# Optimization experiments

Hardware: AMD Instinct MI355X
Metric: run time of the kernel (lower is better)

Reference implementation:

```python
import jax, jax.numpy as jnp
import numpy as np

N_EXPERTS = 8
TOP_K = 2


def setup_inputs() -> dict:
    key = jax.random.key(0)
    ks = jax.random.split(key, 6)
    x = jax.random.normal(ks[0], (4, 2048, 1024), dtype=jnp.float32)
    gate_w = jax.random.normal(ks[1], (8, 1024), dtype=jnp.float32) * 0.02
    w1 = jax.random.normal(ks[2], (8, 4096, 1024), dtype=jnp.float32) * 0.02
    b1 = jax.random.normal(ks[3], (8, 4096), dtype=jnp.float32) * 0.02
    w2 = jax.random.normal(ks[4], (8, 1024, 4096), dtype=jnp.float32) * 0.02
    b2 = jax.random.normal(ks[5], (8, 1024), dtype=jnp.float32) * 0.02
    return {"x": x, "gate_w": gate_w, "w1": w1, "b1": b1, "w2": w2, "b2": b2}


def reference(x, gate_w, w1, b1, w2, b2):
    B, N, C = x.shape
    flat = x.reshape(-1, C)                      # [T, C]
    T = flat.shape[0]
    # Router (eval mode: no noise)
    logits = flat @ gate_w.T                     # [T, E]
    probs = jax.nn.softmax(logits, axis=-1)
    top_p, top_i = jax.lax.top_k(probs, TOP_K)   # [T, K]
    weights = top_p / (jnp.sum(top_p, axis=-1, keepdims=True) + 1e-8)
    # Per-token combine weight per expert: sum_k weights[t,k] * [top_i[t,k]==e]
    combine = jnp.zeros((T, N_EXPERTS), dtype=flat.dtype)
    combine = combine.at[jnp.arange(T)[:, None], top_i].add(weights)  # [T, E]
    # Expert FFNs: small fixed loop over experts, masked-weighted combine.
    out = jnp.zeros_like(flat)
    for e in range(N_EXPERTS):
        h = jax.nn.gelu(flat @ w1[e].T + b1[e])  # [T, H]
        y = h @ w2[e].T + b2[e]                  # [T, C]
        out = out + combine[:, e:e + 1] * y
    return out.reshape(B, N, C)
```

## Files before the change

kernel.cpp:

```cpp
#include <hip/hip_runtime.h>
#include <math.h>

#define T_TOK 8192
#define CD 1024
#define HD 4096
#define NE 8
#define MAX_SLOTS 18432

#define BM 128
#define BN 128
#define BK 64
#define MSLOTS 64
#define G1_NB 32
#define G2_NB 8

typedef __bf16 bf16x8 __attribute__((ext_vector_type(8)));
typedef float f32x4 __attribute__((ext_vector_type(4)));

__device__ __forceinline__ unsigned short f2bf(float f) {
  union { float f; unsigned int u; } v; v.f = f;
  unsigned int u = v.u;
  return (unsigned short)((u + 0x7FFFu + ((u >> 16) & 1u)) >> 16);
}

__device__ __forceinline__ float gelu_fast(float x) {
  float x3 = x * x * x;
  float z = 0.7978845608028654f * (x + 0.044715f * x3);
  float ez = __expf(-2.0f * z);
  return x * __builtin_amdgcn_rcpf(1.0f + ez);
}

__device__ __forceinline__ void glds16(const void* g, void* l) {
  __builtin_amdgcn_global_load_lds((__attribute__((address_space(1))) void*)g,
                                   (__attribute__((address_space(3))) void*)l,
                                   16, 0, 0);
}

__global__ void router_kernel(const float* __restrict__ x, const float* __restrict__ gw,
                              int* __restrict__ meta, int* __restrict__ route_e,
                              float* __restrict__ route_w) {
  __shared__ float4 sgw4[NE * (CD / 4)];
  __shared__ int hist[NE];
  const int tid = threadIdx.x;
  for (int idx = tid; idx < NE * CD / 4; idx += 256) sgw4[idx] = ((const float4*)gw)[idx];
  if (tid < NE) hist[tid] = 0;
  __syncthreads();
  const int wave = tid >> 6, lane = tid & 63;
  const int t0 = blockIdx.x * 16 + wave * 4;
#pragma unroll
  for (int tt = 0; tt < 4; tt++) {
    const int t = t0 + tt;
    const float4* xr4 = (const float4*)(x + (size_t)t * CD);
    float4 xv[4];
#pragma unroll
    for (int it = 0; it < 4; it++) xv[it] = xr4[it * 64 + lane];
    float acc[NE];
#pragma unroll
    for (int e = 0; e < NE; e++) acc[e] = 0.f;
#pragma unroll
    for (int it = 0; it < 4; it++) {
#pragma unroll
      for (int e = 0; e < NE; e++) {
        float4 g = sgw4[e * 256 + it * 64 + lane];
        acc[e] += xv[it].x * g.x + xv[it].y * g.y + xv[it].z * g.z + xv[it].w * g.w;
      }
    }
#pragma unroll
    for (int e = 0; e < NE; e++) {
      float v = acc[e];
#pragma unroll
      for (int off = 32; off > 0; off >>= 1) v += __shfl_xor(v, off);
      acc[e] = v;
    }
    if (lane == 0) {
      float mx = acc[0];
#pragma unroll
      for (int e = 1; e < NE; e++) mx = fmaxf(mx, acc[e]);
      float p[NE], s = 0.f;
#pragma unroll
      for (int e = 0; e < NE; e++) { p[e] = __expf(acc[e] - mx); s += p[e]; }
      float inv = 1.0f / s;
#pragma unroll
      for (int e = 0; e < NE; e++) p[e] *= inv;
      int i0 = 0;
#pragma unroll
      for (int e = 1; e < NE; e++) if (p[e] > p[i0]) i0 = e;
      int i1 = (i0 == 0) ? 1 : 0;
#pragma unroll
      for (int e = 0; e < NE; e++) if (e != i0 && p[e] > p[i1]) i1 = e;
      float den = p[i0] + p[i1] + 1e-8f;
      route_e[t * 2 + 0] = i0; route_e[t * 2 + 1] = i1;
      route_w[t * 2 + 0] = p[i0] / den; route_w[t * 2 + 1] = p[i1] / den;
      atomicAdd(&hist[i0], 1);
      atomicAdd(&hist[i1], 1);
    }
  }
  __syncthreads();
  if (tid < NE && hist[tid] > 0) atomicAdd(&meta[tid], hist[tid]);
}

__global__ void offsets_kernel(int* meta) {
  if (threadIdx.x == 0 && blockIdx.x == 0) {
    int off = 0;
    for (int e = 0; e < NE; e++) {
      int pc = (meta[e] + 255) & ~255;
      meta[8 + e] = off;
      meta[16 + e] = pc;
      off += pc;
    }
  }
}

__global__ void scatter_kernel(const int* __restrict__ route_e, const float* __restrict__ route_w,
                               int* __restrict__ meta, int* __restrict__ slot_token,
                               int* __restrict__ tok_slot) {
  __shared__ int hist[NE], base[NE];
  const int tid = threadIdx.x;
  const int t = blockIdx.x * 256 + tid;
  if (tid < NE) hist[tid] = 0;
  __syncthreads();
  int e0 = route_e[t * 2 + 0], e1 = route_e[t * 2 + 1];
  int lr0 = atomicAdd(&hist[e0], 1);
  int lr1 = atomicAdd(&hist[e1], 1);
  __syncthreads();
  if (tid < NE) base[tid] = (hist[tid] > 0) ? atomicAdd(&meta[24 + tid], hist[tid]) : 0;
  __syncthreads();
  int s0 = meta[8 + e0] + base[e0] + lr0;
  int s1 = meta[8 + e1] + base[e1] + lr1;
  slot_token[s0] = t;
  slot_token[s1] = t;
  tok_slot[t * 2 + 0] = s0;
  tok_slot[t * 2 + 1] = s1;
}

__global__ void gather_kernel(const float* __restrict__ x, const int* __restrict__ slot_token,
                              unsigned short* __restrict__ xg) {
  int slot = blockIdx.x;
  int tkn = slot_token[slot];
  int i = threadIdx.x * 4;
  ushort4 o;
  if (tkn < 0) {
    o.x = 0; o.y = 0; o.z = 0; o.w = 0;
  } else {
    const float4 v = *(const float4*)(x + (size_t)tkn * CD + i);
    o.x = f2bf(v.x); o.y = f2bf(v.y); o.z = f2bf(v.z); o.w = f2bf(v.w);
  }
  *(ushort4*)(xg + (size_t)slot * CD + i) = o;
}

__global__ void cvt_kernel(const float* __restrict__ src, unsigned short* __restrict__ dst, int n4) {
  int i = blockIdx.x * 256 + threadIdx.x;
  if (i >= n4) return;
  const float4 v = *(const float4*)(src + (size_t)i * 4);
  ushort4 o;
  o.x = f2bf(v.x); o.y = f2bf(v.y); o.z = f2bf(v.z); o.w = f2bf(v.w);
  *(ushort4*)(dst + (size_t)i * 4) = o;
}

__global__ __launch_bounds__(256, 3)
void gemm1_kernel(const unsigned short* __restrict__ Ag,
                  const unsigned short* __restrict__ W1,
                  const float* __restrict__ b1,
                  unsigned short* __restrict__ Hout,
                  const int* __restrict__ meta) {
  const int gid = blockIdx.x;
  const int e = gid & 7;
  const int rr = gid >> 3;
  const int sup = rr >> 4;
  const int mi = rr & 3, ni = (rr >> 2) & 3;
  const int m_idx = (sup & 15) * 4 + mi;
  const int n_idx = (sup >> 4) * 4 + ni;
  const int mpad = meta[16 + e];
  const int m0 = m_idx * BM;
  if (m0 >= mpad) return;
  const int n0 = n_idx * BN;
  const int off = meta[8 + e];
  const unsigned short* A = Ag + (size_t)(off + m0) * CD;
  const unsigned short* B = W1 + (size_t)e * (HD * CD) + (size_t)n0 * CD;
  const float* bias = b1 + (size_t)e * HD;

  __shared__ unsigned short As[BM * BK];
  __shared__ unsigned short Bs[BN * BK];
  const int tid = threadIdx.x;
  const int lane = tid & 63, wave = tid >> 6;
  const int wm = wave >> 1, wn = wave & 1;
  const int r = lane & 15, qq = lane >> 4;
  const int lr = lane >> 3;
  const int gc = (lane & 7) ^ lr;
  const int rx = r & 7;

  f32x4 acc[4][4];
#pragma unroll
  for (int i = 0; i < 4; i++)
#pragma unroll
    for (int j = 0; j < 4; j++) acc[i][j] = 0.f;

  for (int kt = 0; kt < CD / BK; kt++) {
#pragma unroll
    for (int c = 0; c < 4; c++) {
      const int rowb = wave * 32 + c * 8;
      glds16(A + (size_t)(rowb + lr) * CD + kt * BK + gc * 8, &As[rowb * BK]);
      glds16(B + (size_t)(rowb + lr) * CD + kt * BK + gc * 8, &Bs[rowb * BK]);
    }
    __syncthreads();
#pragma unroll
    for (int s = 0; s < 2; s++) {
      const int go = (((s << 2) | qq) ^ rx) << 3;
      bf16x8 af[4], bfr[4];
#pragma unroll
      for (int i = 0; i < 4; i++)
        af[i] = *(const bf16x8*)&As[(wm * 64 + i * 16 + r) * BK + go];
#pragma unroll
      for (int j = 0; j < 4; j++)
        bfr[j] = *(const bf16x8*)&Bs[(wn * 64 + j * 16 + r) * BK + go];
#pragma unroll
      for (int i = 0; i < 4; i++)
#pragma unroll
        for (int j = 0; j < 4; j++)
          acc[i][j] = __builtin_amdgcn_mfma_f32_16x16x32_bf16(af[i], bfr[j], acc[i][j], 0, 0, 0);
    }
    __syncthreads();
  }
#pragma unroll
  for (int j = 0; j < 4; j++) {
    int n = n0 + wn * 64 + j * 16 + r;
    float bj = bias[n];
#pragma unroll
    for (int i = 0; i < 4; i++) {
#pragma unroll
      for (int g = 0; g < 4; g++) {
        int ml = wm * 64 + i * 16 + qq * 4 + g;
        Hout[(size_t)(off + m0 + ml) * HD + n] = f2bf(gelu_fast(acc[i][j][g] + bj));
      }
    }
  }
}

__global__ __launch_bounds__(256, 3)
void gemm2_kernel(const unsigned short* __restrict__ Hin,
                  const unsigned short* __restrict__ W2,
                  const float* __restrict__ b2,
                  const int* __restrict__ meta,
                  float* __restrict__ Y) {
  const int gid = blockIdx.x;
  const int e = gid & 7;
  const int rr = gid >> 3;
  const int sup = rr >> 4;
  const int mi = rr & 3, ni = (rr >> 2) & 3;
  const int m_idx = (sup & 15) * 4 + mi;
  const int n_idx = (sup >> 4) * 4 + ni;
  const int mpad = meta[16 + e];
  const int m0 = m_idx * BM;
  if (m0 >= mpad) return;
  const int n0 = n_idx * BN;
  const int off = meta[8 + e];
  const unsigned short* A = Hin + (size_t)(off + m0) * HD;
  const unsigned short* B = W2 + (size_t)e * (CD * HD) + (size_t)n0 * HD;
  const float* bias = b2 + (size_t)e * CD;

  __shared__ unsigned short As[BM * BK];
  __shared__ unsigned short Bs[BN * BK];
  const int tid = threadIdx.x;
  const int lane = tid & 63, wave = tid >> 6;
  const int wm = wave >> 1, wn = wave & 1;
  const int r = lane & 15, qq = lane >> 4;
  const int lr = lane >> 3;
  const int gc = (lane & 7) ^ lr;
  const int rx = r & 7;

  f32x4 acc[4][4];
#pragma unroll
  for (int i = 0; i < 4; i++)
#pragma unroll
    for (int j = 0; j < 4; j++) acc[i][j] = 0.f;

  for (int kt = 0; kt < HD / BK; kt++) {
#pragma unroll
    for (int c = 0; c < 4; c++) {
      const int rowb = wave * 32 + c * 8;
      glds16(A + (size_t)(rowb + lr) * HD + kt * BK + gc * 8, &As[rowb * BK]);
      glds16(B + (size_t)(rowb + lr) * HD + kt * BK + gc * 8, &Bs[rowb * BK]);
    }
    __syncthreads();
#pragma unroll
    for (int s = 0; s < 2; s++) {
      const int go = (((s << 2) | qq) ^ rx) << 3;
      bf16x8 af[4], bfr[4];
#pragma unroll
      for (int i = 0; i < 4; i++)
        af[i] = *(const bf16x8*)&As[(wm * 64 + i * 16 + r) * BK + go];
#pragma unroll
      for (int j = 0; j < 4; j++)
        bfr[j] = *(const bf16x8*)&Bs[(wn * 64 + j * 16 + r) * BK + go];
#pragma unroll
      for (int i = 0; i < 4; i++)
#pragma unroll
        for (int j = 0; j < 4; j++)
          acc[i][j] = __builtin_amdgcn_mfma_f32_16x16x32_bf16(af[i], bfr[j], acc[i][j], 0, 0, 0);
    }
    __syncthreads();
  }
#pragma unroll
  for (int j = 0; j < 4; j++) {
    int n = n0 + wn * 64 + j * 16 + r;
    float bj = bias[n];
#pragma unroll
    for (int i = 0; i < 4; i++) {
#pragma unroll
      for (int g = 0; g < 4; g++) {
        int ml = wm * 64 + i * 16 + qq * 4 + g;
        Y[(size_t)(off + m0 + ml) * CD + n] = acc[i][j][g] + bj;
      }
    }
  }
}

__global__ void combine_kernel(const float* __restrict__ Y, const int* __restrict__ tok_slot,
                               const float* __restrict__ route_w, float* __restrict__ out) {
  const int t = blockIdx.x;
  const int i = threadIdx.x;
  const int s0 = tok_slot[t * 2 + 0], s1 = tok_slot[t * 2 + 1];
  const float w0 = route_w[t * 2 + 0], w1v = route_w[t * 2 + 1];
  const float4 a = ((const float4*)(Y + (size_t)s0 * CD))[i];
  const float4 b = ((const float4*)(Y + (size_t)s1 * CD))[i];
  float4 o;
  o.x = w0 * a.x + w1v * b.x;
  o.y = w0 * a.y + w1v * b.y;
  o.z = w0 * a.z + w1v * b.z;
  o.w = w0 * a.w + w1v * b.w;
  ((float4*)(out + (size_t)t * CD))[i] = o;
}

extern "C" void kernel_launch(void* const* d_in, const int* in_sizes, int n_in,
                              void* d_out, int out_size, void* d_ws, size_t ws_size,
                              hipStream_t stream) {
  const float* x  = (const float*)d_in[0];
  const float* gw = (const float*)d_in[1];
  const float* w1 = (const float*)d_in[2];
  const float* b1 = (const float*)d_in[3];
  const float* w2 = (const float*)d_in[4];
  const float* b2 = (const float*)d_in[5];
  float* out = (float*)d_out;

  char* p = (char*)d_ws;
  size_t o = 0;
  int* meta = (int*)p;                   o = 256;
  int* slot_token = (int*)(p + o);       o += (size_t)MAX_SLOTS * 4;
  int* tok_slot = (int*)(p + o);         o += (size_t)T_TOK * 8;
  int* route_e = (int*)(p + o);          o += (size_t)T_TOK * 8;
  float* route_w = (float*)(p + o);      o += (size_t)T_TOK * 8;
  o = (o + 255) & ~(size_t)255;
  unsigned short* xg  = (unsigned short*)(p + o); o += (size_t)MAX_SLOTS * CD * 2;
  unsigned short* w1b = (unsigned short*)(p + o); o += (size_t)NE * HD * CD * 2;
  unsigned short* w2b = (unsigned short*)(p + o); o += (size_t)NE * CD * HD * 2;
  unsigned short* h   = (unsigned short*)(p + o); o += (size_t)MAX_SLOTS * HD * 2;
  if (ws_size < o) return;
  float* Y = (float*)xg;

  hipMemsetAsync(meta, 0, 256, stream);
  hipMemsetAsync(slot_token, 0xFF, (size_t)MAX_SLOTS * 4, stream);

  router_kernel<<<T_TOK / 16, 256, 0, stream>>>(x, gw, meta, route_e, route_w);
  offsets_kernel<<<1, 64, 0, stream>>>(meta);
  scatter_kernel<<<T_TOK / 256, 256, 0, stream>>>(route_e, route_w, meta, slot_token, tok_slot);
  gather_kernel<<<MAX_SLOTS, 256, 0, stream>>>(x, slot_token, xg);

  const int n4w = NE * HD * CD / 4;
  cvt_kernel<<<n4w / 256, 256, 0, stream>>>(w1, w1b, n4w);
  cvt_kernel<<<n4w / 256, 256, 0, stream>>>(w2, w2b, n4w);

  gemm1_kernel<<<NE * MSLOTS * G1_NB, 256, 0, stream>>>(xg, w1b, b1, h, meta);
  gemm2_kernel<<<NE * MSLOTS * G2_NB, 256, 0, stream>>>(h, w2b, b2, meta, Y);
  combine_kernel<<<T_TOK, 256, 0, stream>>>(Y, tok_slot, route_w, out);
}
```

Measured before the change: 721.7 us.

## Use 256x256 double-buffered MFMA tiles with 512 threads and merge weight conversion

Both expert GEMMs move from 128x128 single-buffered tiles with 256 threads to 256x256 tiles with 512 threads (8 waves). The K loop is double-buffered in LDS, so the next tile's loads are issued during the current MFMA work, and s_setprio raises priority around the MFMA section. The larger tile is meant to raise arithmetic intensity per LDS byte and hide global load latency. The cost is 128 KB of LDS and 128 accumulator registers per lane, which lowers occupancy and leaves more wasted work on partially filled expert tiles. The two weight-conversion launches are also merged into one kernel.

New measurement: 1.008 ms. +39.7%, slower.

```diff
diff --git a/kernel.cpp b/kernel.cpp
--- a/kernel.cpp
+++ b/kernel.cpp
@@ -7,12 +7,9 @@
 #define NE 8
 #define MAX_SLOTS 18432
 
-#define BM 128
-#define BN 128
-#define BK 64
-#define MSLOTS 64
-#define G1_NB 32
-#define G2_NB 8
+#define TB 256
+#define TK 64
+#define MB36 36
 
 typedef __bf16 bf16x8 __attribute__((ext_vector_type(8)));
 typedef float f32x4 __attribute__((ext_vector_type(4)));
@@ -148,16 +145,20 @@
   *(ushort4*)(xg + (size_t)slot * CD + i) = o;
 }
 
-__global__ void cvt_kernel(const float* __restrict__ src, unsigned short* __restrict__ dst, int n4) {
+__global__ void cvtw_kernel(const float* __restrict__ w1, const float* __restrict__ w2,
+                            unsigned short* __restrict__ d1, unsigned short* __restrict__ d2) {
+  const int n4 = NE * HD * CD / 4;
   int i = blockIdx.x * 256 + threadIdx.x;
-  if (i >= n4) return;
-  const float4 v = *(const float4*)(src + (size_t)i * 4);
+  const float* s; unsigned short* d;
+  if (i < n4) { s = w1; d = d1; }
+  else        { s = w2; d = d2; i -= n4; }
+  const float4 v = *(const float4*)(s + (size_t)i * 4);
   ushort4 o;
   o.x = f2bf(v.x); o.y = f2bf(v.y); o.z = f2bf(v.z); o.w = f2bf(v.w);
-  *(ushort4*)(dst + (size_t)i * 4) = o;
-}
-
-__global__ __launch_bounds__(256, 3)
+  *(ushort4*)(d + (size_t)i * 4) = o;
+}
+
+__global__ __launch_bounds__(512, 2)
 void gemm1_kernel(const unsigned short* __restrict__ Ag,
                   const unsigned short* __restrict__ W1,
                   const float* __restrict__ b1,
@@ -166,77 +167,120 @@
   const int gid = blockIdx.x;
   const int e = gid & 7;
   const int rr = gid >> 3;
+  const int mi = rr & 3, ni = (rr >> 2) & 3;
   const int sup = rr >> 4;
-  const int mi = rr & 3, ni = (rr >> 2) & 3;
-  const int m_idx = (sup & 15) * 4 + mi;
-  const int n_idx = (sup >> 4) * 4 + ni;
+  const int msup = sup % 9, nsup = sup / 9;
+  const int m_idx = msup * 4 + mi;
+  const int n_idx = nsup * 4 + ni;
   const int mpad = meta[16 + e];
-  const int m0 = m_idx * BM;
+  const int m0 = m_idx * TB;
   if (m0 >= mpad) return;
-  const int n0 = n_idx * BN;
+  const int n0 = n_idx * TB;
   const int off = meta[8 + e];
   const unsigned short* A = Ag + (size_t)(off + m0) * CD;
   const unsigned short* B = W1 + (size_t)e * (HD * CD) + (size_t)n0 * CD;
   const float* bias = b1 + (size_t)e * HD;
 
-  __shared__ unsigned short As[BM * BK];
-  __shared__ unsigned short Bs[BN * BK];
+  __shared__ unsigned short As[2][TB * TK];
+  __shared__ unsigned short Bs[2][TB * TK];
+
   const int tid = threadIdx.x;
   const int lane = tid & 63, wave = tid >> 6;
-  const int wm = wave >> 1, wn = wave & 1;
-  const int r = lane & 15, qq = lane >> 4;
-  const int lr = lane >> 3;
-  const int gc = (lane & 7) ^ lr;
-  const int rx = r & 7;
-
-  f32x4 acc[4][4];
-#pragma unroll
-  for (int i = 0; i < 4; i++)
+  const int wm = wave >> 2, wn = wave & 3;
+  const int r = lane & 15, qq = lane >> 4, rx = r & 7;
+  const int lr = lane >> 3, lc = lane & 7;
+  const int gc = lc ^ lr;
+
+  const unsigned short* pA[4]; const unsigned short* pB[4]; int dOff[4];
+#pragma unroll
+  for (int c = 0; c < 4; c++) {
+    const int row = c * 64 + wave * 8 + lr;
+    pA[c] = A + (size_t)row * CD + gc * 8;
+    pB[c] = B + (size_t)row * CD + gc * 8;
+    dOff[c] = (c * 64 + wave * 8) * TK;
+  }
+  const int aBase = (wm * 128 + r) * TK;
+  const int bBase = (wn * 64 + r) * TK;
+  const int g0 = (qq ^ rx) << 3;
+  const int g1 = ((4 | qq) ^ rx) << 3;
+
+  f32x4 acc[8][4];
+#pragma unroll
+  for (int i = 0; i < 8; i++)
 #pragma unroll
     for (int j = 0; j < 4; j++) acc[i][j] = 0.f;
 
-  for (int kt = 0; kt < CD / BK; kt++) {
-#pragma unroll
-    for (int c = 0; c < 4; c++) {
-      const int rowb = wave * 32 + c * 8;
-      glds16(A + (size_t)(rowb + lr) * CD + kt * BK + gc * 8, &As[rowb * BK]);
-      glds16(B + (size_t)(rowb + lr) * CD + kt * BK + gc * 8, &Bs[rowb * BK]);
-    }
-    __syncthreads();
-#pragma unroll
-    for (int s = 0; s < 2; s++) {
-      const int go = (((s << 2) | qq) ^ rx) << 3;
-      bf16x8 af[4], bfr[4];
+#pragma unroll
+  for (int c = 0; c < 4; c++) glds16(pA[c], &As[0][dOff[c]]);
+#pragma unroll
+  for (int c = 0; c < 4; c++) glds16(pB[c], &Bs[0][dOff[c]]);
+  asm volatile("s_waitcnt vmcnt(0)" ::: "memory");
+  __syncthreads();
+
+  const int NKT = CD / TK;
+  for (int kt = 0; kt < NKT; kt++) {
+    const int cur = kt & 1;
+    const unsigned short* Ab = &As[cur][0];
+    const unsigned short* Bb = &Bs[cur][0];
+    unsigned short* AsN = &As[cur ^ 1][0];
+    unsigned short* BsN = &Bs[cur ^ 1][0];
+    const bool pf = (kt + 1 < NKT);
+    const size_t ko = (size_t)(kt + 1) * TK;
+#pragma unroll
+    for (int q = 0; q < 4; q++) {
+      if (pf) {
+        if (q == 0) {
+          glds16(pA[0] + ko, AsN + dOff[0]); glds16(pA[1] + ko, AsN + dOff[1]);
+          glds16(pA[2] + ko, AsN + dOff[2]); glds16(pA[3] + ko, AsN + dOff[3]);
+        } else if (q == 1) {
+          glds16(pB[0] + ko, BsN + dOff[0]); glds16(pB[1] + ko, BsN + dOff[1]);
+          glds16(pB[2] + ko, BsN + dOff[2]); glds16(pB[3] + ko, BsN + dOff[3]);
+        }
+      }
+      const int qm = q >> 1, qn = q & 1;
+      bf16x8 af[4][2], bq[2][2];
+#pragma unroll
+      for (int i = 0; i < 4; i++) {
+        af[i][0] = *(const bf16x8*)&Ab[aBase + (qm * 4 + i) * (16 * TK) + g0];
+        af[i][1] = *(const bf16x8*)&Ab[aBase + (qm * 4 + i) * (16 * TK) + g1];
+      }
+#pragma unroll
+      for (int j = 0; j < 2; j++) {
+        bq[j][0] = *(const bf16x8*)&Bb[bBase + (qn * 2 + j) * (16 * TK) + g0];
+        bq[j][1] = *(const bf16x8*)&Bb[bBase + (qn * 2 + j) * (16 * TK) + g1];
+      }
+      __builtin_amdgcn_s_setprio(1);
 #pragma unroll
       for (int i = 0; i < 4; i++)
-        af[i] = *(const bf16x8*)&As[(wm * 64 + i * 16 + r) * BK + go];
-#pragma unroll
-      for (int j = 0; j < 4; j++)
-        bfr[j] = *(const bf16x8*)&Bs[(wn * 64 + j * 16 + r) * BK + go];
-#pragma unroll
-      for (int i = 0; i < 4; i++)
-#pragma unroll
-        for (int j = 0; j < 4; j++)
-          acc[i][j] = __builtin_amdgcn_mfma_f32_16x16x32_bf16(af[i], bfr[j], acc[i][j], 0, 0, 0);
-    }
-    __syncthreads();
-  }
+#pragma unroll
+        for (int j = 0; j < 2; j++) {
+          acc[qm * 4 + i][qn * 2 + j] = __builtin_amdgcn_mfma_f32_16x16x32_bf16(
+              af[i][0], bq[j][0], acc[qm * 4 + i][qn * 2 + j], 0, 0, 0);
+          acc[qm * 4 + i][qn * 2 + j] = __builtin_amdgcn_mfma_f32_16x16x32_bf16(
+              af[i][1], bq[j][1], acc[qm * 4 + i][qn * 2 + j], 0, 0, 0);
+        }
+      __builtin_amdgcn_s_setprio(0);
+      if (q == 3) asm volatile("s_waitcnt vmcnt(0)" ::: "memory");
+      __syncthreads();
+    }
+  }
+  const int orow0 = off + m0 + wm * 128 + qq * 4;
 #pragma unroll
   for (int j = 0; j < 4; j++) {
-    int n = n0 + wn * 64 + j * 16 + r;
-    float bj = bias[n];
-#pragma unroll
-    for (int i = 0; i < 4; i++) {
+    const int n = n0 + wn * 64 + j * 16 + r;
+    const float bj = bias[n];
+#pragma unroll
+    for (int i = 0; i < 8; i++) {
 #pragma unroll
       for (int g = 0; g < 4; g++) {
-        int ml = wm * 64 + i * 16 + qq * 4 + g;
-        Hout[(size_t)(off + m0 + ml) * HD + n] = f2bf(gelu_fast(acc[i][j][g] + bj));
-      }
-    }
-  }
-}
-
-__global__ __launch_bounds__(256, 3)
+        const int row = orow0 + i * 16 + g;
+        Hout[(size_t)row * HD + n] = f2bf(gelu_fast(acc[i][j][g] + bj));
+      }
+    }
+  }
+}
+
+__global__ __launch_bounds__(512, 2)
 void gemm2_kernel(const unsigned short* __restrict__ Hin,
                   const unsigned short* __restrict__ W2,
                   const float* __restrict__ b2,
@@ -245,71 +289,113 @@
   const int gid = blockIdx.x;
   const int e = gid & 7;
   const int rr = gid >> 3;
+  const int mi = rr & 3, ni = (rr >> 2) & 3;
   const int sup = rr >> 4;
-  const int mi = rr & 3, ni = (rr >> 2) & 3;
-  const int m_idx = (sup & 15) * 4 + mi;
-  const int n_idx = (sup >> 4) * 4 + ni;
+  const int m_idx = sup * 4 + mi;
+  const int n_idx = ni;
   const int mpad = meta[16 + e];
-  const int m0 = m_idx * BM;
+  const int m0 = m_idx * TB;
   if (m0 >= mpad) return;
-  const int n0 = n_idx * BN;
+  const int n0 = n_idx * TB;
   const int off = meta[8 + e];
   const unsigned short* A = Hin + (size_t)(off + m0) * HD;
   const unsigned short* B = W2 + (size_t)e * (CD * HD) + (size_t)n0 * HD;
   const float* bias = b2 + (size_t)e * CD;
 
-  __shared__ unsigned short As[BM * BK];
-  __shared__ unsigned short Bs[BN * BK];
+  __shared__ unsigned short As[2][TB * TK];
+  __shared__ unsigned short Bs[2][TB * TK];
+
   const int tid = threadIdx.x;
   const int lane = tid & 63, wave = tid >> 6;
-  const int wm = wave >> 1, wn = wave & 1;
-  const int r = lane & 15, qq = lane >> 4;
-  const int lr = lane >> 3;
-  const int gc = (lane & 7) ^ lr;
-  const int rx = r & 7;
-
-  f32x4 acc[4][4];
-#pragma unroll
-  for (int i = 0; i < 4; i++)
+  const int wm = wave >> 2, wn = wave & 3;
+  const int r = lane & 15, qq = lane >> 4, rx = r & 7;
+  const int lr = lane >> 3, lc = lane & 7;
+  const int gc = lc ^ lr;
+
+  const unsigned short* pA[4]; const unsigned short* pB[4]; int dOff[4];
+#pragma unroll
+  for (int c = 0; c < 4; c++) {
+    const int row = c * 64 + wave * 8 + lr;
+    pA[c] = A + (size_t)row * HD + gc * 8;
+    pB[c] = B + (size_t)row * HD + gc * 8;
+    dOff[c] = (c * 64 + wave * 8) * TK;
+  }
+  const int aBase = (wm * 128 + r) * TK;
+  const int bBase = (wn * 64 + r) * TK;
+  const int g0 = (qq ^ rx) << 3;
+  const int g1 = ((4 | qq) ^ rx) << 3;
+
+  f32x4 acc[8][4];
+#pragma unroll
+  for (int i = 0; i < 8; i++)
 #pragma unroll
     for (int j = 0; j < 4; j++) acc[i][j] = 0.f;
 
-  for (int kt = 0; kt < HD / BK; kt++) {
-#pragma unroll
-    for (int c = 0; c < 4; c++) {
-      const int rowb = wave * 32 + c * 8;
-      glds16(A + (size_t)(rowb + lr) * HD + kt * BK + gc * 8, &As[rowb * BK]);
-      glds16(B + (size_t)(rowb + lr) * HD + kt * BK + gc * 8, &Bs[rowb * BK]);
-    }
-    __syncthreads();
-#pragma unroll
-    for (int s = 0; s < 2; s++) {
-      const int go = (((s << 2) | qq) ^ rx) << 3;
-      bf16x8 af[4], bfr[4];
+#pragma unroll
+  for (int c = 0; c < 4; c++) glds16(pA[c], &As[0][dOff[c]]);
+#pragma unroll
+  for (int c = 0; c < 4; c++) glds16(pB[c], &Bs[0][dOff[c]]);
+  asm volatile("s_waitcnt vmcnt(0)" ::: "memory");
+  __syncthreads();
+
+  const int NKT = HD / TK;
+  for (int kt = 0; kt < NKT; kt++) {
+    const int cur = kt & 1;
+    const unsigned short* Ab = &As[cur][0];
+    const unsigned short* Bb = &Bs[cur][0];
+    unsigned short* AsN = &As[cur ^ 1][0];
+    unsigned short* BsN = &Bs[cur ^ 1][0];
+    const bool pf = (kt + 1 < NKT);
+    const size_t ko = (size_t)(kt + 1) * TK;
+#pragma unroll
+    for (int q = 0; q < 4; q++) {
+      if (pf) {
+        if (q == 0) {
+          glds16(pA[0] + ko, AsN + dOff[0]); glds16(pA[1] + ko, AsN + dOff[1]);
+          glds16(pA[2] + ko, AsN + dOff[2]); glds16(pA[3] + ko, AsN + dOff[3]);
+        } else if (q == 1) {
+          glds16(pB[0] + ko, BsN + dOff[0]); glds16(pB[1] + ko, BsN + dOff[1]);
+          glds16(pB[2] + ko, BsN + dOff[2]); glds16(pB[3] + ko, BsN + dOff[3]);
+        }
+      }
+      const int qm = q >> 1, qn = q & 1;
+      bf16x8 af[4][2], bq[2][2];
+#pragma unroll
+      for (int i = 0; i < 4; i++) {
+        af[i][0] = *(const bf16x8*)&Ab[aBase + (qm * 4 + i) * (16 * TK) + g0];
+        af[i][1] = *(const bf16x8*)&Ab[aBase + (qm * 4 + i) * (16 * TK) + g1];
+      }
+#pragma unroll
+      for (int j = 0; j < 2; j++) {
+        bq[j][0] = *(const bf16x8*)&Bb[bBase + (qn * 2 + j) * (16 * TK) + g0];
+        bq[j][1] = *(const bf16x8*)&Bb[bBase + (qn * 2 + j) * (16 * TK) + g1];
+      }
+      __builtin_amdgcn_s_setprio(1);
 #pragma unroll
       for (int i = 0; i < 4; i++)
-        af[i] = *(const bf16x8*)&As[(wm * 64 + i * 16 + r) * BK + go];
-#pragma unroll
-      for (int j = 0; j < 4; j++)
-        bfr[j] = *(const bf16x8*)&Bs[(wn * 64 + j * 16 + r) * BK + go];
-#pragma unroll
-      for (int i = 0; i < 4; i++)
-#pragma unroll
-        for (int j = 0; j < 4; j++)
-          acc[i][j] = __builtin_amdgcn_mfma_f32_16x16x32_bf16(af[i], bfr[j], acc[i][j], 0, 0, 0);
-    }
-    __syncthreads();
-  }
+#pragma unroll
+        for (int j = 0; j < 2; j++) {
+          acc[qm * 4 + i][qn * 2 + j] = __builtin_amdgcn_mfma_f32_16x16x32_bf16(
+              af[i][0], bq[j][0], acc[qm * 4 + i][qn * 2 + j], 0, 0, 0);
+          acc[qm * 4 + i][qn * 2 + j] = __builtin_amdgcn_mfma_f32_16x16x32_bf16(
+              af[i][1], bq[j][1], acc[qm * 4 + i][qn * 2 + j], 0, 0, 0);
+        }
+      __builtin_amdgcn_s_setprio(0);
+      if (q == 3) asm volatile("s_waitcnt vmcnt(0)" ::: "memory");
+      __syncthreads();
+    }
+  }
+  const int orow0 = off + m0 + wm * 128 + qq * 4;
 #pragma unroll
   for (int j = 0; j < 4; j++) {
-    int n = n0 + wn * 64 + j * 16 + r;
-    float bj = bias[n];
-#pragma unroll
-    for (int i = 0; i < 4; i++) {
+    const int n = n0 + wn * 64 + j * 16 + r;
+    const float bj = bias[n];
+#pragma unroll
+    for (int i = 0; i < 8; i++) {
 #pragma unroll
       for (int g = 0; g < 4; g++) {
-        int ml = wm * 64 + i * 16 + qq * 4 + g;
-        Y[(size_t)(off + m0 + ml) * CD + n] = acc[i][j][g] + bj;
+        const int row = orow0 + i * 16 + g;
+        Y[(size_t)row * CD + n] = acc[i][j][g] + bj;
       }
     }
   }
@@ -366,10 +452,9 @@
   gather_kernel<<<MAX_SLOTS, 256, 0, stream>>>(x, slot_token, xg);
 
   const int n4w = NE * HD * CD / 4;
-  cvt_kernel<<<n4w / 256, 256, 0, stream>>>(w1, w1b, n4w);
-  cvt_kernel<<<n4w / 256, 256, 0, stream>>>(w2, w2b, n4w);
-
-  gemm1_kernel<<<NE * MSLOTS * G1_NB, 256, 0, stream>>>(xg, w1b, b1, h, meta);
-  gemm2_kernel<<<NE * MSLOTS * G2_NB, 256, 0, stream>>>(h, w2b, b2, meta, Y);
+  cvtw_kernel<<<2 * n4w / 256, 256, 0, stream>>>(w1, w2, w1b, w2b);
+
+  gemm1_kernel<<<NE * MB36 * 16, 512, 0, stream>>>(xg, w1b, b1, h, meta);
+  gemm2_kernel<<<NE * MB36 * 4, 512, 0, stream>>>(h, w2b, b2, meta, Y);
   combine_kernel<<<T_TOK, 256, 0, stream>>>(Y, tok_slot, route_w, out);
 }
```

## Triple-buffer GEMM K-loop with async prefetch, 256x128 tiles, 512 threads

Applied to the files above, without the earlier changes.

Both expert GEMMs now use 256x128 tiles with 8 waves and a three-stage LDS ring buffer. Global-to-LDS loads for tile t+2 are issued while MFMAs run on tile t, and each iteration needs only one barrier, gated by explicit vmcnt waits. MFMA sections are wrapped in s_setprio. The two weight conversions are merged into one launch. The larger tiles and 1-block-per-CU launch bounds cut occupancy and raise LDS use in exchange for more reuse and overlap.

Result: slower. 986.4 us (+36.7%).

```diff
diff --git a/kernel.cpp b/kernel.cpp
--- a/kernel.cpp
+++ b/kernel.cpp
@@ -7,12 +7,10 @@
 #define NE 8
 #define MAX_SLOTS 18432
 
-#define BM 128
+#define BM 256
 #define BN 128
-#define BK 64
-#define MSLOTS 64
-#define G1_NB 32
-#define G2_NB 8
+#define TK 64
+#define MB36 36
 
 typedef __bf16 bf16x8 __attribute__((ext_vector_type(8)));
 typedef float f32x4 __attribute__((ext_vector_type(4)));
@@ -148,16 +146,20 @@
   *(ushort4*)(xg + (size_t)slot * CD + i) = o;
 }
 
-__global__ void cvt_kernel(const float* __restrict__ src, unsigned short* __restrict__ dst, int n4) {
+__global__ void cvtw_kernel(const float* __restrict__ w1, const float* __restrict__ w2,
+                            unsigned short* __restrict__ d1, unsigned short* __restrict__ d2) {
+  const int n4 = NE * HD * CD / 4;
   int i = blockIdx.x * 256 + threadIdx.x;
-  if (i >= n4) return;
-  const float4 v = *(const float4*)(src + (size_t)i * 4);
+  const float* s; unsigned short* d;
+  if (i < n4) { s = w1; d = d1; }
+  else        { s = w2; d = d2; i -= n4; }
+  const float4 v = *(const float4*)(s + (size_t)i * 4);
   ushort4 o;
   o.x = f2bf(v.x); o.y = f2bf(v.y); o.z = f2bf(v.z); o.w = f2bf(v.w);
-  *(ushort4*)(dst + (size_t)i * 4) = o;
-}
-
-__global__ __launch_bounds__(256, 3)
+  *(ushort4*)(d + (size_t)i * 4) = o;
+}
+
+__global__ __launch_bounds__(512, 1)
 void gemm1_kernel(const unsigned short* __restrict__ Ag,
                   const unsigned short* __restrict__ W1,
                   const float* __restrict__ b1,
@@ -166,10 +168,11 @@
   const int gid = blockIdx.x;
   const int e = gid & 7;
   const int rr = gid >> 3;
+  const int mi = rr & 3, ni = (rr >> 2) & 3;
   const int sup = rr >> 4;
-  const int mi = rr & 3, ni = (rr >> 2) & 3;
-  const int m_idx = (sup & 15) * 4 + mi;
-  const int n_idx = (sup >> 4) * 4 + ni;
+  const int msup = sup % 9, nsup = sup / 9;
+  const int m_idx = msup * 4 + mi;
+  const int n_idx = nsup * 4 + ni;
   const int mpad = meta[16 + e];
   const int m0 = m_idx * BM;
   if (m0 >= mpad) return;
@@ -179,15 +182,30 @@
   const unsigned short* B = W1 + (size_t)e * (HD * CD) + (size_t)n0 * CD;
   const float* bias = b1 + (size_t)e * HD;
 
-  __shared__ unsigned short As[BM * BK];
-  __shared__ unsigned short Bs[BN * BK];
+  __shared__ unsigned short As[3][BM * TK];
+  __shared__ unsigned short Bs[3][BN * TK];
+
   const int tid = threadIdx.x;
   const int lane = tid & 63, wave = tid >> 6;
   const int wm = wave >> 1, wn = wave & 1;
-  const int r = lane & 15, qq = lane >> 4;
-  const int lr = lane >> 3;
-  const int gc = (lane & 7) ^ lr;
-  const int rx = r & 7;
+  const int r = lane & 15, qq = lane >> 4, rx = r & 7;
+  const int lr = lane >> 3, lc = lane & 7;
+  const int gc = lc ^ lr;
+
+  const unsigned short* pA[4]; int dA[4];
+#pragma unroll
+  for (int c = 0; c < 4; c++) {
+    const int row = c * 64 + wave * 8 + lr;
+    pA[c] = A + (size_t)row * CD + gc * 8;
+    dA[c] = (c * 64 + wave * 8) * TK;
+  }
+  const unsigned short* pB[2]; int dB[2];
+#pragma unroll
+  for (int c = 0; c < 2; c++) {
+    const int row = c * 64 + wave * 8 + lr;
+    pB[c] = B + (size_t)row * CD + gc * 8;
+    dB[c] = (c * 64 + wave * 8) * TK;
+  }
 
   f32x4 acc[4][4];
 #pragma unroll
@@ -195,48 +213,84 @@
 #pragma unroll
     for (int j = 0; j < 4; j++) acc[i][j] = 0.f;
 
-  for (int kt = 0; kt < CD / BK; kt++) {
-#pragma unroll
-    for (int c = 0; c < 4; c++) {
-      const int rowb = wave * 32 + c * 8;
-      glds16(A + (size_t)(rowb + lr) * CD + kt * BK + gc * 8, &As[rowb * BK]);
-      glds16(B + (size_t)(rowb + lr) * CD + kt * BK + gc * 8, &Bs[rowb * BK]);
-    }
-    __syncthreads();
+#pragma unroll
+  for (int c = 0; c < 4; c++) glds16(pA[c], &As[0][dA[c]]);
+#pragma unroll
+  for (int c = 0; c < 2; c++) glds16(pB[c], &Bs[0][dB[c]]);
+#pragma unroll
+  for (int c = 0; c < 4; c++) glds16(pA[c] + TK, &As[1][dA[c]]);
+#pragma unroll
+  for (int c = 0; c < 2; c++) glds16(pB[c] + TK, &Bs[1][dB[c]]);
+  asm volatile("s_waitcnt vmcnt(6)" ::: "memory");
+  __builtin_amdgcn_s_barrier();
+  asm volatile("" ::: "memory");
+  __builtin_amdgcn_sched_barrier(0);
+
+  const int NKT = CD / TK;
+  int cur = 0;
+  for (int t = 0; t < NKT; t++) {
+    const int n2 = (cur >= 1) ? cur - 1 : 2;
+    const unsigned short* Ab = &As[cur][0];
+    const unsigned short* Bb = &Bs[cur][0];
+    unsigned short* An = &As[n2][0];
+    unsigned short* Bn = &Bs[n2][0];
+    const bool pf = (t + 2 < NKT);
+    const size_t ko = (size_t)(t + 2) * TK;
 #pragma unroll
     for (int s = 0; s < 2; s++) {
+      if (pf) {
+        if (s == 0) {
+          glds16(pA[0] + ko, An + dA[0]);
+          glds16(pA[1] + ko, An + dA[1]);
+          glds16(pB[0] + ko, Bn + dB[0]);
+        } else {
+          glds16(pA[2] + ko, An + dA[2]);
+          glds16(pA[3] + ko, An + dA[3]);
+          glds16(pB[1] + ko, Bn + dB[1]);
+        }
+      }
       const int go = (((s << 2) | qq) ^ rx) << 3;
-      bf16x8 af[4], bfr[4];
+      bf16x8 af[4], bf[4];
 #pragma unroll
       for (int i = 0; i < 4; i++)
-        af[i] = *(const bf16x8*)&As[(wm * 64 + i * 16 + r) * BK + go];
+        af[i] = *(const bf16x8*)&Ab[(wm * 64 + i * 16 + r) * TK + go];
 #pragma unroll
       for (int j = 0; j < 4; j++)
-        bfr[j] = *(const bf16x8*)&Bs[(wn * 64 + j * 16 + r) * BK + go];
+        bf[j] = *(const bf16x8*)&Bb[(wn * 64 + j * 16 + r) * TK + go];
+      __builtin_amdgcn_s_setprio(1);
 #pragma unroll
       for (int i = 0; i < 4; i++)
 #pragma unroll
         for (int j = 0; j < 4; j++)
-          acc[i][j] = __builtin_amdgcn_mfma_f32_16x16x32_bf16(af[i], bfr[j], acc[i][j], 0, 0, 0);
-    }
-    __syncthreads();
-  }
+          acc[i][j] = __builtin_amdgcn_mfma_f32_16x16x32_bf16(af[i], bf[j], acc[i][j], 0, 0, 0);
+      __builtin_amdgcn_s_setprio(0);
+    }
+    if (t < NKT - 1) {
+      if (pf) asm volatile("s_waitcnt vmcnt(6)" ::: "memory");
+      else    asm volatile("s_waitcnt vmcnt(0)" ::: "memory");
+      __builtin_amdgcn_s_barrier();
+      asm volatile("" ::: "memory");
+      __builtin_amdgcn_sched_barrier(0);
+    }
+    cur = (cur == 2) ? 0 : cur + 1;
+  }
+  const int orow0 = off + m0 + wm * 64 + qq * 4;
 #pragma unroll
   for (int j = 0; j < 4; j++) {
-    int n = n0 + wn * 64 + j * 16 + r;
-    float bj = bias[n];
+    const int n = n0 + wn * 64 + j * 16 + r;
+    const float bj = bias[n];
 #pragma unroll
     for (int i = 0; i < 4; i++) {
 #pragma unroll
       for (int g = 0; g < 4; g++) {
-        int ml = wm * 64 + i * 16 + qq * 4 + g;
-        Hout[(size_t)(off + m0 + ml) * HD + n] = f2bf(gelu_fast(acc[i][j][g] + bj));
+        const int row = orow0 + i * 16 + g;
+        Hout[(size_t)row * HD + n] = f2bf(gelu_fast(acc[i][j][g] + bj));
       }
     }
   }
 }
 
-__global__ __launch_bounds__(256, 3)
+__global__ __launch_bounds__(512, 1)
 void gemm2_kernel(const unsigned short* __restrict__ Hin,
                   const unsigned short* __restrict__ W2,
                   const float* __restrict__ b2,
@@ -245,10 +299,11 @@
   const int gid = blockIdx.x;
   const int e = gid & 7;
   const int rr = gid >> 3;
+  const int mi = rr & 3, ni = (rr >> 2) & 3;
   const int sup = rr >> 4;
-  const int mi = rr & 3, ni = (rr >> 2) & 3;
-  const int m_idx = (sup & 15) * 4 + mi;
-  const int n_idx = (sup >> 4) * 4 + ni;
+  const int msup = sup % 9, nsup = sup / 9;
+  const int m_idx = msup * 4 + mi;
+  const int n_idx = nsup * 4 + ni;
   const int mpad = meta[16 + e];
   const int m0 = m_idx * BM;
   if (m0 >= mpad) return;
@@ -258,15 +313,30 @@
   const unsigned short* B = W2 + (size_t)e * (CD * HD) + (size_t)n0 * HD;
   const float* bias = b2 + (size_t)e * CD;
 
-  __shared__ unsigned short As[BM * BK];
-  __shared__ unsigned short Bs[BN * BK];
+  __shared__ unsigned short As[3][BM * TK];
+  __shared__ unsigned short Bs[3][BN * TK];
+
   const int tid = threadIdx.x;
   const int lane = tid & 63, wave = tid >> 6;
   const int wm = wave >> 1, wn = wave & 1;
-  const int r = lane & 15, qq = lane >> 4;
-  const int lr = lane >> 3;
-  const int gc = (lane & 7) ^ lr;
-  const int rx = r & 7;
+  const int r = lane & 15, qq = lane >> 4, rx = r & 7;
+  const int lr = lane >> 3, lc = lane & 7;
+  const int gc = lc ^ lr;
+
+  const unsigned short* pA[4]; int dA[4];
+#pragma unroll
+  for (int c = 0; c < 4; c++) {
+    const int row = c * 64 + wave * 8 + lr;
+    pA[c] = A + (size_t)row * HD + gc * 8;
+    dA[c] = (c * 64 + wave * 8) * TK;
+  }
+  const unsigned short* pB[2]; int dB[2];
+#pragma unroll
+  for (int c = 0; c < 2; c++) {
+    const int row = c * 64 + wave * 8 + lr;
+    pB[c] = B + (size_t)row * HD + gc * 8;
+    dB[c] = (c * 64 + wave * 8) * TK;
+  }
 
   f32x4 acc[4][4];
 #pragma unroll
@@ -274,42 +344,78 @@
 #pragma unroll
     for (int j = 0; j < 4; j++) acc[i][j] = 0.f;
 
-  for (int kt = 0; kt < HD / BK; kt++) {
-#pragma unroll
-    for (int c = 0; c < 4; c++) {
-      const int rowb = wave * 32 + c * 8;
-      glds16(A + (size_t)(rowb + lr) * HD + kt * BK + gc * 8, &As[rowb * BK]);
-      glds16(B + (size_t)(rowb + lr) * HD + kt * BK + gc * 8, &Bs[rowb * BK]);
-    }
-    __syncthreads();
+#pragma unroll
+  for (int c = 0; c < 4; c++) glds16(pA[c], &As[0][dA[c]]);
+#pragma unroll
+  for (int c = 0; c < 2; c++) glds16(pB[c], &Bs[0][dB[c]]);
+#pragma unroll
+  for (int c = 0; c < 4; c++) glds16(pA[c] + TK, &As[1][dA[c]]);
+#pragma unroll
+  for (int c = 0; c < 2; c++) glds16(pB[c] + TK, &Bs[1][dB[c]]);
+  asm volatile("s_waitcnt vmcnt(6)" ::: "memory");
+  __builtin_amdgcn_s_barrier();
+  asm volatile("" ::: "memory");
+  __builtin_amdgcn_sched_barrier(0);
+
+  const int NKT = HD / TK;
+  int cur = 0;
+  for (int t = 0; t < NKT; t++) {
+    const int n2 = (cur >= 1) ? cur - 1 : 2;
+    const unsigned short* Ab = &As[cur][0];
+    const unsigned short* Bb = &Bs[cur][0];
+    unsigned short* An = &As[n2][0];
+    unsigned short* Bn = &Bs[n2][0];
+    const bool pf = (t + 2 < NKT);
+    const size_t ko = (size_t)(t + 2) * TK;
 #pragma unroll
     for (int s = 0; s < 2; s++) {
+      if (pf) {
+        if (s == 0) {
+          glds16(pA[0] + ko, An + dA[0]);
+          glds16(pA[1] + ko, An + dA[1]);
+          glds16(pB[0] + ko, Bn + dB[0]);
+        } else {
+          glds16(pA[2] + ko, An + dA[2]);
+          glds16(pA[3] + ko, An + dA[3]);
+          glds16(pB[1] + ko, Bn + dB[1]);
+        }
+      }
       const int go = (((s << 2) | qq) ^ rx) << 3;
-      bf16x8 af[4], bfr[4];
+      bf16x8 af[4], bf[4];
 #pragma unroll
       for (int i = 0; i < 4; i++)
-        af[i] = *(const bf16x8*)&As[(wm * 64 + i * 16 + r) * BK + go];
+        af[i] = *(const bf16x8*)&Ab[(wm * 64 + i * 16 + r) * TK + go];
 #pragma unroll
       for (int j = 0; j < 4; j++)
-        bfr[j] = *(const bf16x8*)&Bs[(wn * 64 + j * 16 + r) * BK + go];
+        bf[j] = *(const bf16x8*)&Bb[(wn * 64 + j * 16 + r) * TK + go];
+      __builtin_amdgcn_s_setprio(1);
 #pragma unroll
       for (int i = 0; i < 4; i++)
 #pragma unroll
         for (int j = 0; j < 4; j++)
-          acc[i][j] = __builtin_amdgcn_mfma_f32_16x16x32_bf16(af[i], bfr[j], acc[i][j], 0, 0, 0);
-    }
-    __syncthreads();
-  }
+          acc[i][j] = __builtin_amdgcn_mfma_f32_16x16x32_bf16(af[i], bf[j], acc[i][j], 0, 0, 0);
+      __builtin_amdgcn_s_setprio(0);
+    }
+    if (t < NKT - 1) {
+      if (pf) asm volatile("s_waitcnt vmcnt(6)" ::: "memory");
+      else    asm volatile("s_waitcnt vmcnt(0)" ::: "memory");
+      __builtin_amdgcn_s_barrier();
+      asm volatile("" ::: "memory");
+      __builtin_amdgcn_sched_barrier(0);
+    }
+    cur = (cur == 2) ? 0 : cur + 1;
+  }
+  const int orow0 = off + m0 + wm * 64 + qq * 4;
 #pragma unroll
   for (int j = 0; j < 4; j++) {
-    int n = n0 + wn * 64 + j * 16 + r;
-    float bj = bias[n];
+    const int n = n0 + wn * 64 + j * 16 + r;
+    const float bj = bias[n];
 #pragma unroll
     for (int i = 0; i < 4; i++) {
 #pragma unroll
       for (int g = 0; g < 4; g++) {
-        int ml = wm * 64 + i * 16 + qq * 4 + g;
-        Y[(size_t)(off + m0 + ml) * CD + n] = acc[i][j][g] + bj;
+        const int row = orow0 + i * 16 + g;
+        Y[(size_t)row * CD + n] = acc[i][j][g] + bj;
       }
     }
   }
@@ -366,10 +472,9 @@
   gather_kernel<<<MAX_SLOTS, 256, 0, stream>>>(x, slot_token, xg);
 
   const int n4w = NE * HD * CD / 4;
-  cvt_kernel<<<n4w / 256, 256, 0, stream>>>(w1, w1b, n4w);
-  cvt_kernel<<<n4w / 256, 256, 0, stream>>>(w2, w2b, n4w);
-
-  gemm1_kernel<<<NE * MSLOTS * G1_NB, 256, 0, stream>>>(xg, w1b, b1, h, meta);
-  gemm2_kernel<<<NE * MSLOTS * G2_NB, 256, 0, stream>>>(h, w2b, b2, meta, Y);
+  cvtw_kernel<<<2 * n4w / 256, 256, 0, stream>>>(w1, w2, w1b, w2b);
+
+  gemm1_kernel<<<NE * MB36 * 32, 512, 0, stream>>>(xg, w1b, b1, h, meta);
+  gemm2_kernel<<<NE * MB36 * 8, 512, 0, stream>>>(h, w2b, b2, meta, Y);
   combine_kernel<<<T_TOK, 256, 0, stream>>>(Y, tok_slot, route_w, out);
 }
```
